# Kernel tuning notes

Hardware: AMD Instinct MI355X
Metric: run time of the kernel (lower is better)

Reference implementation:

```python
import jax, jax.numpy as jnp
import numpy as np

EMBED_DIM = 1024
NUM_HEADS = 16
HEAD_DIM = EMBED_DIM // NUM_HEADS
SCALE = HEAD_DIM ** -0.5


def setup_inputs() -> dict:
    key = jax.random.key(0)
    ks = jax.random.split(key, 12)
    B, S, D = 2, 2048, EMBED_DIM
    w_std = D ** -0.5
    return {
        "query": jax.random.normal(ks[0], (B, S, D), jnp.float32),
        "key": jax.random.normal(ks[1], (B, S, D), jnp.float32),
        "value": jax.random.normal(ks[2], (B, S, D), jnp.float32),
        "mask": jnp.ones((B, S, S), jnp.int32),
        "Wq": jax.random.normal(ks[3], (D, D), jnp.float32) * w_std,
        "bq": jnp.zeros((D,), jnp.float32),
        "Wk": jax.random.normal(ks[4], (D, D), jnp.float32) * w_std,
        "bk": jnp.zeros((D,), jnp.float32),
        "Wv": jax.random.normal(ks[5], (D, D), jnp.float32) * w_std,
        "bv": jnp.zeros((D,), jnp.float32),
        "Wo": jax.random.normal(ks[6], (D, D), jnp.float32) * w_std,
        "bo": jnp.zeros((D,), jnp.float32),
    }


def reference(query, key, value, mask, Wq, bq, Wk, bk, Wv, bv, Wo, bo):
    B, Sq, D = query.shape
    H, Hd = NUM_HEADS, HEAD_DIM
    # projections (torch Linear: x @ W.T + b), then split heads -> [B, H, S, Hd]
    q = (query @ Wq.T + bq).reshape(B, Sq, H, Hd).transpose(0, 2, 1, 3)
    k = (key @ Wk.T + bk).reshape(B, -1, H, Hd).transpose(0, 2, 1, 3)
    v = (value @ Wv.T + bv).reshape(B, -1, H, Hd).transpose(0, 2, 1, 3)
    # scaled dot-product scores [B, H, Sq, Sk]
    scores = jnp.einsum("bhqd,bhkd->bhqk", q, k) * SCALE
    scores = jnp.where(mask[:, None, :, :] == 0, -1e9, scores)
    attn_weights = jax.nn.softmax(scores, axis=-1)
    # dropout rate = 0.0 -> identity in this configuration
    attn_output = jnp.einsum("bhqk,bhkd->bhqd", attn_weights, v)
    attn_output = attn_output.transpose(0, 2, 1, 3).reshape(B, Sq, D)
    output = attn_output @ Wo.T + bo
    return (output, attn_weights)
```

## Files before the change

kernel.cpp:

```cpp
#include <hip/hip_runtime.h>
#include <stdint.h>

#define B_ 2
#define S_ 2048
#define D_ 1024
#define H_ 16
#define HD_ 64
#define NT_ (S_ / 64)
#define SC2_ 0.18033688011112042f

typedef __bf16 bf16_t;
typedef bf16_t bf16x8 __attribute__((ext_vector_type(8)));
typedef float f32x4 __attribute__((ext_vector_type(4)));
typedef unsigned short u16x8 __attribute__((ext_vector_type(8)));
typedef unsigned short u16x4 __attribute__((ext_vector_type(4)));

static __device__ __forceinline__ unsigned short f2b(float f) {
  return __builtin_bit_cast(unsigned short, (bf16_t)f);
}

static __device__ __forceinline__ bf16x8 asb(u16x8 u) {
  return __builtin_bit_cast(bf16x8, u);
}

__global__ void cast3(const float* __restrict__ a, const float* __restrict__ b,
                      const float* __restrict__ c,
                      unsigned short* __restrict__ dst, int n) {
  const float* src = blockIdx.y == 0 ? a : (blockIdx.y == 1 ? b : c);
  unsigned short* d = dst + (size_t)blockIdx.y * n;
  int i = (blockIdx.x * blockDim.x + threadIdx.x) * 8;
  if (i >= n) return;
  float4 f0 = *(const float4*)(src + i);
  float4 f1 = *(const float4*)(src + i + 4);
  u16x8 o;
  o[0] = f2b(f0.x); o[1] = f2b(f0.y); o[2] = f2b(f0.z); o[3] = f2b(f0.w);
  o[4] = f2b(f1.x); o[5] = f2b(f1.y); o[6] = f2b(f1.z); o[7] = f2b(f1.w);
  *(u16x8*)(d + i) = o;
}

__global__ void cast4(const float* __restrict__ a, const float* __restrict__ b,
                      const float* __restrict__ c, const float* __restrict__ e,
                      unsigned short* __restrict__ dst, int n) {
  const float* src = blockIdx.y == 0 ? a
                   : (blockIdx.y == 1 ? b : (blockIdx.y == 2 ? c : e));
  unsigned short* d = dst + (size_t)blockIdx.y * n;
  int i = (blockIdx.x * blockDim.x + threadIdx.x) * 8;
  if (i >= n) return;
  float4 f0 = *(const float4*)(src + i);
  float4 f1 = *(const float4*)(src + i + 4);
  u16x8 o;
  o[0] = f2b(f0.x); o[1] = f2b(f0.y); o[2] = f2b(f0.z); o[3] = f2b(f0.w);
  o[4] = f2b(f1.x); o[5] = f2b(f1.y); o[6] = f2b(f1.z); o[7] = f2b(f1.w);
  *(u16x8*)(d + i) = o;
}

__global__ void pack_mask(const int* __restrict__ mask,
                          uint32_t* __restrict__ mbits) {
  int i = blockIdx.x * blockDim.x + threadIdx.x;
  unsigned long long bits = __ballot(mask[i] != 0);
  if ((threadIdx.x & 63) == 0)
    *(unsigned long long*)&mbits[i >> 5] = bits;
}

template<int OUTMODE>
__global__ __launch_bounds__(256)
void gemm_bt(const unsigned short* __restrict__ Ab,
             const unsigned short* __restrict__ Wb,
             const float* __restrict__ bq_,
             const float* __restrict__ bk_,
             const float* __restrict__ bv_,
             void* __restrict__ outv,
             int M, int N, int K) {
  const int z = blockIdx.z;
  const unsigned short* A = Ab + (size_t)z * M * K;
  const unsigned short* W = Wb + (size_t)z * N * K;
  const float* bias = z == 0 ? bq_ : (z == 1 ? bk_ : bv_);

  __shared__ __align__(16) unsigned short As[128 * 40];
  __shared__ __align__(16) unsigned short Bs[128 * 40];

  const int tid = threadIdx.x;
  const int lane = tid & 63;
  const int wave = tid >> 6;
  const int wm = wave >> 1, wn = wave & 1;
  const int row0 = blockIdx.x * 128;
  const int col0 = blockIdx.y * 128;

  const int srow = tid >> 2;
  const int scol = (tid & 3) * 8;
  const int lr = lane & 15;
  const int lg = lane >> 4;
  const int lk = lg * 8;

  f32x4 acc[4][4] = {};

  u16x8 a0 = *(const u16x8*)&A[(size_t)(row0 + srow) * K + scol];
  u16x8 a1 = *(const u16x8*)&A[(size_t)(row0 + srow + 64) * K + scol];
  u16x8 b0 = *(const u16x8*)&W[(size_t)(col0 + srow) * K + scol];
  u16x8 b1 = *(const u16x8*)&W[(size_t)(col0 + srow + 64) * K + scol];

  for (int k0 = 0; k0 < K; k0 += 32) {
    __syncthreads();
    *(u16x8*)&As[srow * 40 + scol] = a0;
    *(u16x8*)&As[(srow + 64) * 40 + scol] = a1;
    *(u16x8*)&Bs[srow * 40 + scol] = b0;
    *(u16x8*)&Bs[(srow + 64) * 40 + scol] = b1;
    if (k0 + 32 < K) {
      a0 = *(const u16x8*)&A[(size_t)(row0 + srow) * K + k0 + 32 + scol];
      a1 = *(const u16x8*)&A[(size_t)(row0 + srow + 64) * K + k0 + 32 + scol];
      b0 = *(const u16x8*)&W[(size_t)(col0 + srow) * K + k0 + 32 + scol];
      b1 = *(const u16x8*)&W[(size_t)(col0 + srow + 64) * K + k0 + 32 + scol];
    }
    __syncthreads();

    bf16x8 af[4], bfr[4];
#pragma unroll
    for (int i = 0; i < 4; ++i)
      af[i] = asb(*(const u16x8*)&As[(wm * 64 + i * 16 + lr) * 40 + lk]);
#pragma unroll
    for (int j = 0; j < 4; ++j)
      bfr[j] = asb(*(const u16x8*)&Bs[(wn * 64 + j * 16 + lr) * 40 + lk]);
#pragma unroll
    for (int i = 0; i < 4; ++i)
#pragma unroll
      for (int j = 0; j < 4; ++j)
        acc[i][j] = __builtin_amdgcn_mfma_f32_16x16x32_bf16(af[i], bfr[j], acc[i][j], 0, 0, 0);
  }

  const size_t zo = (size_t)z * M * N;
#pragma unroll
  for (int i = 0; i < 4; ++i) {
#pragma unroll
    for (int j = 0; j < 4; ++j) {
      const int row_ = row0 + wm * 64 + i * 16 + lg * 4;
      const int col = col0 + wn * 64 + j * 16 + lr;
      const float bcol = bias[col];
      if (OUTMODE == 1) {
        float* O = (float*)outv;
#pragma unroll
        for (int r = 0; r < 4; ++r)
          __builtin_nontemporal_store(acc[i][j][r] + bcol,
                                      &O[(size_t)(row_ + r) * N + col]);
      } else if (z == 2) {
        unsigned short* O = (unsigned short*)outv + zo;
        int b = row_ >> 11, s = row_ & 2047;
        int h = col >> 6, hd = col & 63;
        u16x4 pk;
#pragma unroll
        for (int r = 0; r < 4; ++r) pk[r] = f2b(acc[i][j][r] + bcol);
        *(u16x4*)&O[(((size_t)b * H_ + h) * HD_ + hd) * S_ + s] = pk;
      } else {
        unsigned short* O = (unsigned short*)outv + zo;
        int h = col >> 6, hd = col & 63;
#pragma unroll
        for (int r = 0; r < 4; ++r) {
          int row = row_ + r;
          int b = row >> 11, s = row & 2047;
          O[(((size_t)b * H_ + h) * S_ + s) * HD_ + hd] = f2b(acc[i][j][r] + bcol);
        }
      }
    }
  }
}

__global__ __launch_bounds__(512)
void attn_pass1(const unsigned short* __restrict__ q_bh,
                const unsigned short* __restrict__ k_bh,
                const uint32_t* __restrict__ mbits,
                float2* __restrict__ ml) {
  const int bh = blockIdx.y;
  const int b = bh >> 4;
  const int q0 = blockIdx.x * 128;

  __shared__ __align__(16) unsigned short Ks[64 * 72];

  const int tid = threadIdx.x, lane = tid & 63, wave = tid >> 6;
  const int srow = tid >> 3, scol = (tid & 7) * 8;
  const int lr = lane & 15, lg = lane >> 4, lk = lg * 8;
  const int sq = q0 + wave * 16 + lr;

  const unsigned short* qb = q_bh + ((size_t)bh * S_ + sq) * HD_;
  bf16x8 qf0 = asb(*(const u16x8*)&qb[lk]);
  bf16x8 qf1 = asb(*(const u16x8*)&qb[32 + lk]);

  const uint32_t* mrow = mbits + ((size_t)b * S_ + sq) * (S_ / 32);
  const unsigned short* kb = k_bh + (size_t)bh * S_ * HD_;

  float m2 = -__builtin_inff(), l = 0.f;

  u16x8 t0 = *(const u16x8*)&kb[srow * 64 + scol];

  for (int kt = 0; kt < NT_; ++kt) {
    __syncthreads();
    *(u16x8*)&Ks[srow * 72 + scol] = t0;
    if (kt + 1 < NT_) {
      const unsigned short* kn = kb + (kt + 1) * 64 * 64;
      t0 = *(const u16x8*)&kn[srow * 64 + scol];
    }
    __syncthreads();

    uint2 mw = *(const uint2*)&mrow[kt * 2];
    const bool full = __all((mw.x & mw.y) == 0xffffffffu);

    f32x4 sa[4] = {};
#pragma unroll
    for (int j = 0; j < 4; ++j) {
      bf16x8 kf0 = asb(*(const u16x8*)&Ks[(j * 16 + lr) * 72 + lk]);
      bf16x8 kf1 = asb(*(const u16x8*)&Ks[(j * 16 + lr) * 72 + 32 + lk]);
      sa[j] = __builtin_amdgcn_mfma_f32_16x16x32_bf16(kf0, qf0, sa[j], 0, 0, 0);
      sa[j] = __builtin_amdgcn_mfma_f32_16x16x32_bf16(kf1, qf1, sa[j], 0, 0, 0);
    }

    float sv[4][4];
    if (full) {
#pragma unroll
      for (int j = 0; j < 4; ++j)
#pragma unroll
        for (int r = 0; r < 4; ++r) sv[j][r] = sa[j][r] * SC2_;
    } else {
#pragma unroll
      for (int j = 0; j < 4; ++j) {
        uint32_t mwj = (j < 2) ? mw.x : mw.y;
#pragma unroll
        for (int r = 0; r < 4; ++r) {
          int bit = (j & 1) * 16 + lg * 4 + r;
          sv[j][r] = ((mwj >> bit) & 1) ? sa[j][r] * SC2_ : -3.0e9f;
        }
      }
    }
    float tm = sv[0][0];
#pragma unroll
    for (int j = 0; j < 4; ++j)
#pragma unroll
      for (int r = 0; r < 4; ++r) tm = fmaxf(tm, sv[j][r]);
    tm = fmaxf(tm, __shfl_xor(tm, 16));
    tm = fmaxf(tm, __shfl_xor(tm, 32));
    float mnew = fmaxf(m2, tm);
    float ss = 0.f;
#pragma unroll
    for (int j = 0; j < 4; ++j)
#pragma unroll
      for (int r = 0; r < 4; ++r)
        ss += __builtin_amdgcn_exp2f(sv[j][r] - mnew);
    ss += __shfl_xor(ss, 16);
    ss += __shfl_xor(ss, 32);
    l = l * __builtin_amdgcn_exp2f(m2 - mnew) + ss;
    m2 = mnew;
  }
  if (lg == 0) ml[(size_t)bh * S_ + sq] = make_float2(m2, l);
}

__global__ __launch_bounds__(256)
void attn_pass2(const unsigned short* __restrict__ q_bh,
                const unsigned short* __restrict__ k_bh,
                const unsigned short* __restrict__ vt_g,
                const uint32_t* __restrict__ mbits,
                const float2* __restrict__ ml,
                float* __restrict__ w_out,
                unsigned short* __restrict__ attn_out) {
  const int bh = blockIdx.y;
  const int b = bh >> 4, h = bh & (H_ - 1);
  const int q0 = blockIdx.x * 64;

  __shared__ __align__(16) unsigned short Ks[64 * 72];
  __shared__ __align__(16) unsigned short Vs[64 * 72];
  __shared__ __align__(16) unsigned short Ps[4][16 * 72];

  const int tid = threadIdx.x, lane = tid & 63, wave = tid >> 6;
  const int srow = tid >> 3, scol = (tid & 7) * 8;
  const int lr = lane & 15, lg = lane >> 4, lk = lg * 8;
  const int sq = q0 + wave * 16 + lr;

  const unsigned short* qb = q_bh + ((size_t)bh * S_ + sq) * HD_;
  bf16x8 qf0 = asb(*(const u16x8*)&qb[lk]);
  bf16x8 qf1 = asb(*(const u16x8*)&qb[32 + lk]);

  float2 t = ml[(size_t)bh * S_ + sq];
  const float off = -t.x - __builtin_amdgcn_logf(t.y);
  const uint32_t* mrow = mbits + ((size_t)b * S_ + sq) * (S_ / 32);
  float* wrow = w_out + ((size_t)bh * S_ + sq) * S_;

  const unsigned short* kb = k_bh + (size_t)bh * S_ * HD_;
  const unsigned short* vb = vt_g + (size_t)bh * HD_ * S_;

  u16x8 t0 = *(const u16x8*)&kb[srow * 64 + scol];
  u16x8 t1 = *(const u16x8*)&kb[(srow + 32) * 64 + scol];
  u16x8 v0 = *(const u16x8*)&vb[(size_t)srow * S_ + scol];
  u16x8 v1 = *(const u16x8*)&vb[(size_t)(srow + 32) * S_ + scol];

  f32x4 oacc[4] = {};

  for (int kt = 0; kt < NT_; ++kt) {
    const int k0 = kt * 64;
    __syncthreads();
    *(u16x8*)&Ks[srow * 72 + scol] = t0;
    *(u16x8*)&Ks[(srow + 32) * 72 + scol] = t1;
    *(u16x8*)&Vs[srow * 72 + scol] = v0;
    *(u16x8*)&Vs[(srow + 32) * 72 + scol] = v1;
    if (kt + 1 < NT_) {
      t0 = *(const u16x8*)&kb[(k0 + 64 + srow) * 64 + scol];
      t1 = *(const u16x8*)&kb[(k0 + 64 + srow + 32) * 64 + scol];
      v0 = *(const u16x8*)&vb[(size_t)srow * S_ + k0 + 64 + scol];
      v1 = *(const u16x8*)&vb[(size_t)(srow + 32) * S_ + k0 + 64 + scol];
    }
    __syncthreads();

    uint2 mw = *(const uint2*)&mrow[kt * 2];
    const bool full = __all((mw.x & mw.y) == 0xffffffffu);

    f32x4 sa[4] = {};
#pragma unroll
    for (int j = 0; j < 4; ++j) {
      bf16x8 kf0 = asb(*(const u16x8*)&Ks[(j * 16 + lr) * 72 + lk]);
      bf16x8 kf1 = asb(*(const u16x8*)&Ks[(j * 16 + lr) * 72 + 32 + lk]);
      sa[j] = __builtin_amdgcn_mfma_f32_16x16x32_bf16(kf0, qf0, sa[j], 0, 0, 0);
      sa[j] = __builtin_amdgcn_mfma_f32_16x16x32_bf16(kf1, qf1, sa[j], 0, 0, 0);
    }

#pragma unroll
    for (int j = 0; j < 4; ++j) {
      f32x4 pv;
      u16x4 pb;
      if (full) {
#pragma unroll
        for (int r = 0; r < 4; ++r) {
          float p = __builtin_amdgcn_exp2f(fmaf(sa[j][r], SC2_, off));
          pv[r] = p;
          pb[r] = f2b(p);
        }
      } else {
        uint32_t mwj = (j < 2) ? mw.x : mw.y;
#pragma unroll
        for (int r = 0; r < 4; ++r) {
          int bit = (j & 1) * 16 + lg * 4 + r;
          float x = ((mwj >> bit) & 1) ? fmaf(sa[j][r], SC2_, off) : -3.0e9f;
          float p = __builtin_amdgcn_exp2f(x);
          pv[r] = p;
          pb[r] = f2b(p);
        }
      }
      __builtin_nontemporal_store(pv, (f32x4*)&wrow[k0 + j * 16 + lg * 4]);
      *(u16x4*)&Ps[wave][lr * 72 + j * 16 + lg * 4] = pb;
    }

#pragma unroll
    for (int ks = 0; ks < 2; ++ks) {
      bf16x8 pa = asb(*(const u16x8*)&Ps[wave][lr * 72 + ks * 32 + lk]);
#pragma unroll
      for (int j2 = 0; j2 < 4; ++j2) {
        bf16x8 vf = asb(*(const u16x8*)&Vs[(j2 * 16 + lr) * 72 + ks * 32 + lk]);
        oacc[j2] = __builtin_amdgcn_mfma_f32_16x16x32_bf16(pa, vf, oacc[j2], 0, 0, 0);
      }
    }
  }

#pragma unroll
  for (int j2 = 0; j2 < 4; ++j2)
#pragma unroll
    for (int r = 0; r < 4; ++r)
      attn_out[((size_t)b * S_ + q0 + wave * 16 + lg * 4 + r) * D_ + h * HD_ + j2 * 16 + lr] =
          f2b(oacc[j2][r]);
}

extern "C" void kernel_launch(void* const* d_in, const int* in_sizes, int n_in,
                              void* d_out, int out_size, void* d_ws, size_t ws_size,
                              hipStream_t stream) {
  const float* query = (const float*)d_in[0];
  const float* key   = (const float*)d_in[1];
  const float* value = (const float*)d_in[2];
  const int*   mask  = (const int*)d_in[3];
  const float* Wq = (const float*)d_in[4];
  const float* bq = (const float*)d_in[5];
  const float* Wk = (const float*)d_in[6];
  const float* bk = (const float*)d_in[7];
  const float* Wv = (const float*)d_in[8];
  const float* bv = (const float*)d_in[9];
  const float* Wo = (const float*)d_in[10];
  const float* bo = (const float*)d_in[11];

  const int NE = B_ * S_ * D_;
  const int NW = D_ * D_;

  char* ws = (char*)d_ws;
  unsigned short* xin  = (unsigned short*)(ws);
  uint32_t*       mbits = (uint32_t*)(ws + 8388608);
  unsigned short* wbuf = (unsigned short*)(ws + 25165824);
  unsigned short* qkv  = (unsigned short*)(ws + 33554432);
  float2* mlbuf        = (float2*)(ws + 58720256);
  unsigned short* aout = (unsigned short*)(ws + 59244544);

  cast3<<<dim3(NE / 2048, 3), dim3(256), 0, stream>>>(query, key, value, xin, NE);
  cast4<<<dim3(NW / 2048, 4), dim3(256), 0, stream>>>(Wq, Wk, Wv, Wo, wbuf, NW);

  gemm_bt<0><<<dim3(32, 8, 3), dim3(256), 0, stream>>>(
      xin, wbuf, bq, bk, bv, qkv, 4096, 1024, 1024);

  pack_mask<<<dim3(B_ * S_ * S_ / 256), dim3(256), 0, stream>>>(mask, mbits);

  float* w_out = (float*)d_out + NE;
  attn_pass1<<<dim3(16, 32), dim3(512), 0, stream>>>(qkv, qkv + NE, mbits, mlbuf);
  attn_pass2<<<dim3(32, 32), dim3(256), 0, stream>>>(
      qkv, qkv + NE, qkv + 2 * NE, mbits, mlbuf, w_out, aout);

  gemm_bt<1><<<dim3(32, 8, 1), dim3(256), 0, stream>>>(
      aout, wbuf + 3 * NW, bo, bo, bo, d_out, 4096, 1024, 1024);
}
```

Before: 322.0 us.

## Split key tiles across wave pairs and remap blocks per XCD

Both attention passes now give each 16-row query strip to two waves, each covering half of every 64-key tile. Partial softmax statistics and partial PV accumulators are merged through shared memory at the end. Blocks are remapped so that each XCD handles a contiguous group of heads, which is meant to improve L2 reuse of K/V. This doubles the waves per block and shortens per-wave dependency chains, at the cost of an extra reduction step and more shared memory.

```diff
diff --git a/kernel.cpp b/kernel.cpp
--- a/kernel.cpp
+++ b/kernel.cpp
@@ -163,21 +163,30 @@
   }
 }
 
+static __device__ __forceinline__ void xcd_map(int& bh, int& qt) {
+  int lin = blockIdx.y * 32 + blockIdx.x;
+  int xcd = lin & 7, k = lin >> 3;
+  bh = (xcd << 2) | (k >> 5);
+  qt = k & 31;
+}
+
 __global__ __launch_bounds__(512)
 void attn_pass1(const unsigned short* __restrict__ q_bh,
                 const unsigned short* __restrict__ k_bh,
                 const uint32_t* __restrict__ mbits,
                 float2* __restrict__ ml) {
-  const int bh = blockIdx.y;
+  int bh, qt;
+  xcd_map(bh, qt);
   const int b = bh >> 4;
-  const int q0 = blockIdx.x * 128;
+  const int q0 = qt * 64;
 
   __shared__ __align__(16) unsigned short Ks[64 * 72];
 
-  const int tid = threadIdx.x, lane = tid & 63, wave = tid >> 6;
+  const int tid = threadIdx.x, lane = tid & 63, w = tid >> 6;
+  const int wq = w >> 1, wk = w & 1;
   const int srow = tid >> 3, scol = (tid & 7) * 8;
   const int lr = lane & 15, lg = lane >> 4, lk = lg * 8;
-  const int sq = q0 + wave * 16 + lr;
+  const int sq = q0 + wq * 16 + lr;
 
   const unsigned short* qb = q_bh + ((size_t)bh * S_ + sq) * HD_;
   bf16x8 qf0 = asb(*(const u16x8*)&qb[lk]);
@@ -199,58 +208,68 @@
     }
     __syncthreads();
 
-    uint2 mw = *(const uint2*)&mrow[kt * 2];
-    const bool full = __all((mw.x & mw.y) == 0xffffffffu);
-
-    f32x4 sa[4] = {};
-#pragma unroll
-    for (int j = 0; j < 4; ++j) {
+    uint32_t mw = mrow[kt * 2 + wk];
+    const bool full = __all(mw == 0xffffffffu);
+
+    f32x4 sa[2] = {};
+#pragma unroll
+    for (int jj = 0; jj < 2; ++jj) {
+      const int j = wk * 2 + jj;
       bf16x8 kf0 = asb(*(const u16x8*)&Ks[(j * 16 + lr) * 72 + lk]);
       bf16x8 kf1 = asb(*(const u16x8*)&Ks[(j * 16 + lr) * 72 + 32 + lk]);
-      sa[j] = __builtin_amdgcn_mfma_f32_16x16x32_bf16(kf0, qf0, sa[j], 0, 0, 0);
-      sa[j] = __builtin_amdgcn_mfma_f32_16x16x32_bf16(kf1, qf1, sa[j], 0, 0, 0);
-    }
-
-    float sv[4][4];
+      sa[jj] = __builtin_amdgcn_mfma_f32_16x16x32_bf16(kf0, qf0, sa[jj], 0, 0, 0);
+      sa[jj] = __builtin_amdgcn_mfma_f32_16x16x32_bf16(kf1, qf1, sa[jj], 0, 0, 0);
+    }
+
+    float sv[2][4];
     if (full) {
 #pragma unroll
-      for (int j = 0; j < 4; ++j)
-#pragma unroll
-        for (int r = 0; r < 4; ++r) sv[j][r] = sa[j][r] * SC2_;
+      for (int jj = 0; jj < 2; ++jj)
+#pragma unroll
+        for (int r = 0; r < 4; ++r) sv[jj][r] = sa[jj][r] * SC2_;
     } else {
 #pragma unroll
-      for (int j = 0; j < 4; ++j) {
-        uint32_t mwj = (j < 2) ? mw.x : mw.y;
+      for (int jj = 0; jj < 2; ++jj)
 #pragma unroll
         for (int r = 0; r < 4; ++r) {
-          int bit = (j & 1) * 16 + lg * 4 + r;
-          sv[j][r] = ((mwj >> bit) & 1) ? sa[j][r] * SC2_ : -3.0e9f;
+          int bit = jj * 16 + lg * 4 + r;
+          sv[jj][r] = ((mw >> bit) & 1) ? sa[jj][r] * SC2_ : -3.0e9f;
         }
-      }
     }
     float tm = sv[0][0];
 #pragma unroll
-    for (int j = 0; j < 4; ++j)
-#pragma unroll
-      for (int r = 0; r < 4; ++r) tm = fmaxf(tm, sv[j][r]);
+    for (int jj = 0; jj < 2; ++jj)
+#pragma unroll
+      for (int r = 0; r < 4; ++r) tm = fmaxf(tm, sv[jj][r]);
     tm = fmaxf(tm, __shfl_xor(tm, 16));
     tm = fmaxf(tm, __shfl_xor(tm, 32));
     float mnew = fmaxf(m2, tm);
     float ss = 0.f;
 #pragma unroll
-    for (int j = 0; j < 4; ++j)
+    for (int jj = 0; jj < 2; ++jj)
 #pragma unroll
       for (int r = 0; r < 4; ++r)
-        ss += __builtin_amdgcn_exp2f(sv[j][r] - mnew);
+        ss += __builtin_amdgcn_exp2f(sv[jj][r] - mnew);
     ss += __shfl_xor(ss, 16);
     ss += __shfl_xor(ss, 32);
     l = l * __builtin_amdgcn_exp2f(m2 - mnew) + ss;
     m2 = mnew;
   }
-  if (lg == 0) ml[(size_t)bh * S_ + sq] = make_float2(m2, l);
-}
-
-__global__ __launch_bounds__(256)
+
+  __syncthreads();
+  float2* mls = (float2*)Ks;
+  if (wk == 1 && lg == 0) mls[wq * 16 + lr] = make_float2(m2, l);
+  __syncthreads();
+  if (wk == 0 && lg == 0) {
+    float2 o = mls[wq * 16 + lr];
+    float mn = fmaxf(m2, o.x);
+    float lo = l * __builtin_amdgcn_exp2f(m2 - mn) +
+               o.y * __builtin_amdgcn_exp2f(o.x - mn);
+    ml[(size_t)bh * S_ + sq] = make_float2(mn, lo);
+  }
+}
+
+__global__ __launch_bounds__(512)
 void attn_pass2(const unsigned short* __restrict__ q_bh,
                 const unsigned short* __restrict__ k_bh,
                 const unsigned short* __restrict__ vt_g,
@@ -258,18 +277,23 @@
                 const float2* __restrict__ ml,
                 float* __restrict__ w_out,
                 unsigned short* __restrict__ attn_out) {
-  const int bh = blockIdx.y;
+  int bh, qt;
+  xcd_map(bh, qt);
   const int b = bh >> 4, h = bh & (H_ - 1);
-  const int q0 = blockIdx.x * 64;
-
-  __shared__ __align__(16) unsigned short Ks[64 * 72];
-  __shared__ __align__(16) unsigned short Vs[64 * 72];
-  __shared__ __align__(16) unsigned short Ps[4][16 * 72];
-
-  const int tid = threadIdx.x, lane = tid & 63, wave = tid >> 6;
+  const int q0 = qt * 64;
+
+  __shared__ __align__(16) unsigned char smem[36864];
+  unsigned short* Ks = (unsigned short*)smem;
+  unsigned short* Vs = Ks + 64 * 72;
+  unsigned short* Ps = Vs + 64 * 72;
+  float* cs = (float*)smem;
+
+  const int tid = threadIdx.x, lane = tid & 63, w = tid >> 6;
+  const int wq = w >> 1, wk = w & 1;
   const int srow = tid >> 3, scol = (tid & 7) * 8;
   const int lr = lane & 15, lg = lane >> 4, lk = lg * 8;
-  const int sq = q0 + wave * 16 + lr;
+  const int sq = q0 + wq * 16 + lr;
+  unsigned short* Psw = Ps + w * (16 * 72);
 
   const unsigned short* qb = q_bh + ((size_t)bh * S_ + sq) * HD_;
   bf16x8 qf0 = asb(*(const u16x8*)&qb[lk]);
@@ -284,9 +308,7 @@
   const unsigned short* vb = vt_g + (size_t)bh * HD_ * S_;
 
   u16x8 t0 = *(const u16x8*)&kb[srow * 64 + scol];
-  u16x8 t1 = *(const u16x8*)&kb[(srow + 32) * 64 + scol];
   u16x8 v0 = *(const u16x8*)&vb[(size_t)srow * S_ + scol];
-  u16x8 v1 = *(const u16x8*)&vb[(size_t)(srow + 32) * S_ + scol];
 
   f32x4 oacc[4] = {};
 
@@ -294,72 +316,79 @@
     const int k0 = kt * 64;
     __syncthreads();
     *(u16x8*)&Ks[srow * 72 + scol] = t0;
-    *(u16x8*)&Ks[(srow + 32) * 72 + scol] = t1;
     *(u16x8*)&Vs[srow * 72 + scol] = v0;
-    *(u16x8*)&Vs[(srow + 32) * 72 + scol] = v1;
     if (kt + 1 < NT_) {
       t0 = *(const u16x8*)&kb[(k0 + 64 + srow) * 64 + scol];
-      t1 = *(const u16x8*)&kb[(k0 + 64 + srow + 32) * 64 + scol];
       v0 = *(const u16x8*)&vb[(size_t)srow * S_ + k0 + 64 + scol];
-      v1 = *(const u16x8*)&vb[(size_t)(srow + 32) * S_ + k0 + 64 + scol];
-    }
-    __syncthreads();
-
-    uint2 mw = *(const uint2*)&mrow[kt * 2];
-    const bool full = __all((mw.x & mw.y) == 0xffffffffu);
-
-    f32x4 sa[4] = {};
-#pragma unroll
-    for (int j = 0; j < 4; ++j) {
+    }
+    __syncthreads();
+
+    uint32_t mw = mrow[kt * 2 + wk];
+    const bool full = __all(mw == 0xffffffffu);
+
+    f32x4 sa[2] = {};
+#pragma unroll
+    for (int jj = 0; jj < 2; ++jj) {
+      const int j = wk * 2 + jj;
       bf16x8 kf0 = asb(*(const u16x8*)&Ks[(j * 16 + lr) * 72 + lk]);
       bf16x8 kf1 = asb(*(const u16x8*)&Ks[(j * 16 + lr) * 72 + 32 + lk]);
-      sa[j] = __builtin_amdgcn_mfma_f32_16x16x32_bf16(kf0, qf0, sa[j], 0, 0, 0);
-      sa[j] = __builtin_amdgcn_mfma_f32_16x16x32_bf16(kf1, qf1, sa[j], 0, 0, 0);
-    }
-
-#pragma unroll
-    for (int j = 0; j < 4; ++j) {
+      sa[jj] = __builtin_amdgcn_mfma_f32_16x16x32_bf16(kf0, qf0, sa[jj], 0, 0, 0);
+      sa[jj] = __builtin_amdgcn_mfma_f32_16x16x32_bf16(kf1, qf1, sa[jj], 0, 0, 0);
+    }
+
+#pragma unroll
+    for (int jj = 0; jj < 2; ++jj) {
       f32x4 pv;
       u16x4 pb;
       if (full) {
 #pragma unroll
         for (int r = 0; r < 4; ++r) {
-          float p = __builtin_amdgcn_exp2f(fmaf(sa[j][r], SC2_, off));
+          float p = __builtin_amdgcn_exp2f(fmaf(sa[jj][r], SC2_, off));
           pv[r] = p;
           pb[r] = f2b(p);
         }
       } else {
-        uint32_t mwj = (j < 2) ? mw.x : mw.y;
 #pragma unroll
         for (int r = 0; r < 4; ++r) {
-          int bit = (j & 1) * 16 + lg * 4 + r;
-          float x = ((mwj >> bit) & 1) ? fmaf(sa[j][r], SC2_, off) : -3.0e9f;
+          int bit = jj * 16 + lg * 4 + r;
+          float x = ((mw >> bit) & 1) ? fmaf(sa[jj][r], SC2_, off) : -3.0e9f;
           float p = __builtin_amdgcn_exp2f(x);
           pv[r] = p;
           pb[r] = f2b(p);
         }
       }
-      __builtin_nontemporal_store(pv, (f32x4*)&wrow[k0 + j * 16 + lg * 4]);
-      *(u16x4*)&Ps[wave][lr * 72 + j * 16 + lg * 4] = pb;
-    }
-
-#pragma unroll
-    for (int ks = 0; ks < 2; ++ks) {
-      bf16x8 pa = asb(*(const u16x8*)&Ps[wave][lr * 72 + ks * 32 + lk]);
-#pragma unroll
-      for (int j2 = 0; j2 < 4; ++j2) {
-        bf16x8 vf = asb(*(const u16x8*)&Vs[(j2 * 16 + lr) * 72 + ks * 32 + lk]);
-        oacc[j2] = __builtin_amdgcn_mfma_f32_16x16x32_bf16(pa, vf, oacc[j2], 0, 0, 0);
+      __builtin_nontemporal_store(pv,
+          (f32x4*)&wrow[k0 + wk * 32 + jj * 16 + lg * 4]);
+      *(u16x4*)&Psw[lr * 72 + wk * 32 + jj * 16 + lg * 4] = pb;
+    }
+
+    bf16x8 pa = asb(*(const u16x8*)&Psw[lr * 72 + wk * 32 + lk]);
+#pragma unroll
+    for (int j2 = 0; j2 < 4; ++j2) {
+      bf16x8 vf = asb(*(const u16x8*)&Vs[(j2 * 16 + lr) * 72 + wk * 32 + lk]);
+      oacc[j2] = __builtin_amdgcn_mfma_f32_16x16x32_bf16(pa, vf, oacc[j2], 0, 0, 0);
+    }
+  }
+
+  __syncthreads();
+  const int ci = (wq * 64 + lane) * 17;
+  if (wk == 1) {
+#pragma unroll
+    for (int j2 = 0; j2 < 4; ++j2)
+#pragma unroll
+      for (int r = 0; r < 4; ++r) cs[ci + j2 * 4 + r] = oacc[j2][r];
+  }
+  __syncthreads();
+  if (wk == 0) {
+#pragma unroll
+    for (int j2 = 0; j2 < 4; ++j2)
+#pragma unroll
+      for (int r = 0; r < 4; ++r) {
+        float v = oacc[j2][r] + cs[ci + j2 * 4 + r];
+        attn_out[((size_t)b * S_ + q0 + wq * 16 + lg * 4 + r) * D_ + h * HD_ + j2 * 16 + lr] =
+            f2b(v);
       }
-    }
-  }
-
-#pragma unroll
-  for (int j2 = 0; j2 < 4; ++j2)
-#pragma unroll
-    for (int r = 0; r < 4; ++r)
-      attn_out[((size_t)b * S_ + q0 + wave * 16 + lg * 4 + r) * D_ + h * HD_ + j2 * 16 + lr] =
-          f2b(oacc[j2][r]);
+  }
 }
 
 extern "C" void kernel_launch(void* const* d_in, const int* in_sizes, int n_in,
@@ -398,8 +427,8 @@
   pack_mask<<<dim3(B_ * S_ * S_ / 256), dim3(256), 0, stream>>>(mask, mbits);
 
   float* w_out = (float*)d_out + NE;
-  attn_pass1<<<dim3(16, 32), dim3(512), 0, stream>>>(qkv, qkv + NE, mbits, mlbuf);
-  attn_pass2<<<dim3(32, 32), dim3(256), 0, stream>>>(
+  attn_pass1<<<dim3(32, 32), dim3(512), 0, stream>>>(qkv, qkv + NE, mbits, mlbuf);
+  attn_pass2<<<dim3(32, 32), dim3(512), 0, stream>>>(
       qkv, qkv + NE, qkv + 2 * NE, mbits, mlbuf, w_out, aout);
 
   gemm_bt<1><<<dim3(32, 8, 1), dim3(256), 0, stream>>>(
```

Result: faster. 297.5 us (-7.6%).
